# Kernel optimization log

Measured on AMD Instinct MI355X. Metric: run time of the kernel, lower is better.

The kernel has to match this reference:

```python
import jax, jax.numpy as jnp
import numpy as np

HIDDEN = 1024
HEADS = 16
HEAD_DIM = HIDDEN // HEADS
SCALE = HEAD_DIM ** (-0.5)


def setup_inputs() -> dict:
    key = jax.random.key(0)
    ks = jax.random.split(key, 5)
    B, N, C = 8, 1024, HIDDEN
    x = jax.random.normal(ks[0], (B, N, C), dtype=jnp.float32)
    # torch nn.Linear params: weight [out, in], bias [out]
    w_in = jax.random.normal(ks[1], (3 * C, C), dtype=jnp.float32) * (C ** -0.5)
    b_in = jax.random.normal(ks[2], (3 * C,), dtype=jnp.float32) * 0.02
    w_out = jax.random.normal(ks[3], (C, C), dtype=jnp.float32) * (C ** -0.5)
    b_out = jax.random.normal(ks[4], (C,), dtype=jnp.float32) * 0.02
    return {"x": x, "w_in": w_in, "b_in": b_in, "w_out": w_out, "b_out": b_out}


def reference(x, w_in, b_in, w_out, b_out):
    B, N, C = x.shape
    H, D = HEADS, HEAD_DIM
    # in_proj: [B,N,3C] -> (3,B,H,N,D)
    qkv = x @ w_in.T + b_in
    qkv = qkv.reshape(B, N, 3, H, D).transpose(2, 0, 3, 1, 4)
    q, k, v = qkv[0], qkv[1], qkv[2]
    # attention scores scaled after QK^T (same math as scaling q)
    attn = jnp.einsum("bhnd,bhmd->bhnm", q, k) * SCALE
    attn = jax.nn.softmax(attn, axis=-1)
    out = jnp.einsum("bhnm,bhmd->bhnd", attn, v)  # [B,H,N,D]
    out = out.transpose(0, 2, 1, 3).reshape(B, N, C)
    return out @ w_out.T + b_out
```

## Files before the change

kernel.cpp:

```cpp
#include <hip/hip_runtime.h>


typedef __attribute__((ext_vector_type(8))) __bf16 bf16x8;
typedef __attribute__((ext_vector_type(4))) __bf16 bf16x4;
typedef __attribute__((ext_vector_type(4))) float f32x4;
typedef __attribute__((ext_vector_type(4))) short short4v;

__device__ __forceinline__ f32x4 mfma16(bf16x8 a, bf16x8 b, f32x4 c) {
  return __builtin_amdgcn_mfma_f32_16x16x32_bf16(a, b, c, 0, 0, 0);
}

#if __has_builtin(__builtin_amdgcn_mfma_f32_16x16x16bf16_1k)
__device__ __forceinline__ f32x4 mfma_pv(bf16x4 a, bf16x4 b, f32x4 c) {
  short4v as = __builtin_bit_cast(short4v, a);
  short4v bs = __builtin_bit_cast(short4v, b);
  return __builtin_amdgcn_mfma_f32_16x16x16bf16_1k(as, bs, c, 0, 0, 0);
}
#else
__device__ __forceinline__ f32x4 mfma_pv(bf16x4 a, bf16x4 b, f32x4 c) {
  __bf16 z = (__bf16)0.f;
  bf16x8 a8 = {a[0], a[1], a[2], a[3], z, z, z, z};
  bf16x8 b8 = {b[0], b[1], b[2], b[3], z, z, z, z};
  return mfma16(a8, b8, c);
}
#endif

__device__ __forceinline__ float fexp2(float x) {
#if __has_builtin(__builtin_amdgcn_exp2f)
  return __builtin_amdgcn_exp2f(x);
#else
  return exp2f(x);
#endif
}

typedef __attribute__((address_space(1))) const unsigned int gu32;
typedef __attribute__((address_space(3))) unsigned int lu32;

__device__ __forceinline__ void async16(const void* g, void* l) {
  __builtin_amdgcn_global_load_lds((gu32*)g, (lu32*)l, 16, 0, 0);
}

__global__ __launch_bounds__(256) void cvt_all(const float* __restrict__ x,
                                               __bf16* __restrict__ xb,
                                               const float* __restrict__ wi,
                                               __bf16* __restrict__ wib,
                                               const float* __restrict__ wo,
                                               __bf16* __restrict__ wob) {
  int blk = blockIdx.x;
  const float* in;
  __bf16* out;
  int base;
  if (blk < 4096)      { in = x;  out = xb;  base = 0; }
  else if (blk < 5632) { in = wi; out = wib; base = 4096; }
  else                 { in = wo; out = wob; base = 5632; }
  int i = ((blk - base) * 256 + threadIdx.x) * 8;
  float4 a = *(const float4*)(in + i);
  float4 b = *(const float4*)(in + i + 4);
  bf16x8 o;
  o[0] = (__bf16)a.x; o[1] = (__bf16)a.y; o[2] = (__bf16)a.z; o[3] = (__bf16)a.w;
  o[4] = (__bf16)b.x; o[5] = (__bf16)b.y; o[6] = (__bf16)b.z; o[7] = (__bf16)b.w;
  *(bf16x8*)(out + i) = o;
}

template <int NB, bool WRITE_VT, typename OutT>
__global__ __launch_bounds__(256) void gemm_nt(const __bf16* __restrict__ A,
                                               const __bf16* __restrict__ Bm,
                                               const float* __restrict__ bias,
                                               OutT* __restrict__ C, int K, int ldc,
                                               __bf16* __restrict__ vt) {
  __shared__ __bf16 As[128 * 64];
  __shared__ __bf16 Bs[NB * 32 * 64];
  const int t = threadIdx.x;
  const int wv = t >> 6, lane = t & 63;
  const int q16 = lane & 15, quad = lane >> 4;
  const int wm = wv >> 1, wn = wv & 1;
  const long m0 = (long)blockIdx.x * 128;
  const long n0 = (long)blockIdx.y * (NB * 32);

  f32x4 zero = {0.f, 0.f, 0.f, 0.f};
  f32x4 acc[4][NB];
#pragma unroll
  for (int i = 0; i < 4; ++i)
#pragma unroll
    for (int j = 0; j < NB; ++j) acc[i][j] = zero;

  char* AsB = (char*)As;
  char* BsB = (char*)Bs;
  const int sr = t >> 3;
  const int gc = (t & 7) ^ (sr & 7);

  for (int kt = 0; kt < K; kt += 64) {
    __syncthreads();
#pragma unroll
    for (int i = 0; i < 4; ++i)
      async16(A + (m0 + i * 32 + sr) * K + kt + gc * 8, AsB + i * 4096 + wv * 1024);
#pragma unroll
    for (int i = 0; i < NB; ++i)
      async16(Bm + (n0 + i * 32 + sr) * K + kt + gc * 8, BsB + i * 4096 + wv * 1024);
    __syncthreads();

#pragma unroll
    for (int kk = 0; kk < 2; ++kk) {
      bf16x8 af[4], bf[NB];
#pragma unroll
      for (int i = 0; i < 4; ++i) {
        int ra = wm * 64 + i * 16 + q16;
        af[i] = *(const bf16x8*)(AsB + ra * 128 + (((kk * 4 + quad) ^ (ra & 7)) * 16));
      }
#pragma unroll
      for (int j = 0; j < NB; ++j) {
        int rb = wn * (NB * 16) + j * 16 + q16;
        bf[j] = *(const bf16x8*)(BsB + rb * 128 + (((kk * 4 + quad) ^ (rb & 7)) * 16));
      }
#pragma unroll
      for (int i = 0; i < 4; ++i)
#pragma unroll
        for (int j = 0; j < NB; ++j) acc[i][j] = mfma16(af[i], bf[j], acc[i][j]);
    }
  }

  if (WRITE_VT && n0 >= 2048) {
    const int b = (int)(m0 >> 10);
    const int nbase = (int)(m0 - (long)b * 1024) + wm * 64;
#pragma unroll
    for (int j = 0; j < NB; ++j) {
      int col = (int)n0 + wn * (NB * 16) + j * 16 + q16;
      int cc = col - 2048;
      int h = cc >> 6, d = cc & 63;
      float bs = bias[col];
      __bf16* vrow = vt + (((long)(b * 16 + h)) << 16) + (long)d * 1024;
#pragma unroll
      for (int i = 0; i < 4; ++i) {
        int n = nbase + i * 16 + quad * 4;
        bf16x4 o;
#pragma unroll
        for (int r = 0; r < 4; ++r) o[r] = (__bf16)(acc[i][j][r] + bs);
        *(bf16x4*)(vrow + n) = o;
      }
    }
  } else {
#pragma unroll
    for (int j = 0; j < NB; ++j) {
      long col = n0 + wn * (NB * 16) + j * 16 + q16;
      float bs = bias[col];
#pragma unroll
      for (int i = 0; i < 4; ++i) {
        long rowb = m0 + wm * 64 + i * 16 + quad * 4;
#pragma unroll
        for (int r = 0; r < 4; ++r) {
          float v = acc[i][j][r] + bs;
          C[(rowb + r) * (long)ldc + col] = (OutT)v;
        }
      }
    }
  }
}

template <typename OutT>
__global__ __launch_bounds__(256) void gemm_nt64(const __bf16* __restrict__ A,
                                                 const __bf16* __restrict__ Bm,
                                                 const float* __restrict__ bias,
                                                 OutT* __restrict__ C, int K, int ldc) {
  __shared__ __bf16 As[64 * 64];
  __shared__ __bf16 Bs[128 * 64];
  const int t = threadIdx.x;
  const int wv = t >> 6, lane = t & 63;
  const int q16 = lane & 15, quad = lane >> 4;
  const int wm = wv >> 1, wn = wv & 1;
  const long m0 = (long)blockIdx.x * 64;
  const long n0 = (long)blockIdx.y * 128;

  f32x4 zero = {0.f, 0.f, 0.f, 0.f};
  f32x4 acc[2][4];
#pragma unroll
  for (int i = 0; i < 2; ++i)
#pragma unroll
    for (int j = 0; j < 4; ++j) acc[i][j] = zero;

  char* AsB = (char*)As;
  char* BsB = (char*)Bs;
  const int sr = t >> 3;
  const int gc = (t & 7) ^ (sr & 7);

  for (int kt = 0; kt < K; kt += 64) {
    __syncthreads();
#pragma unroll
    for (int i = 0; i < 2; ++i)
      async16(A + (m0 + i * 32 + sr) * K + kt + gc * 8, AsB + i * 4096 + wv * 1024);
#pragma unroll
    for (int i = 0; i < 4; ++i)
      async16(Bm + (n0 + i * 32 + sr) * K + kt + gc * 8, BsB + i * 4096 + wv * 1024);
    __syncthreads();

#pragma unroll
    for (int kk = 0; kk < 2; ++kk) {
      bf16x8 af[2], bf[4];
#pragma unroll
      for (int i = 0; i < 2; ++i) {
        int ra = wm * 32 + i * 16 + q16;
        af[i] = *(const bf16x8*)(AsB + ra * 128 + (((kk * 4 + quad) ^ (ra & 7)) * 16));
      }
#pragma unroll
      for (int j = 0; j < 4; ++j) {
        int rb = wn * 64 + j * 16 + q16;
        bf[j] = *(const bf16x8*)(BsB + rb * 128 + (((kk * 4 + quad) ^ (rb & 7)) * 16));
      }
#pragma unroll
      for (int i = 0; i < 2; ++i)
#pragma unroll
        for (int j = 0; j < 4; ++j) acc[i][j] = mfma16(af[i], bf[j], acc[i][j]);
    }
  }

#pragma unroll
  for (int j = 0; j < 4; ++j) {
    long col = n0 + wn * 64 + j * 16 + q16;
    float bs = bias[col];
#pragma unroll
    for (int i = 0; i < 2; ++i) {
      long rowb = m0 + wm * 32 + i * 16 + quad * 4;
#pragma unroll
      for (int r = 0; r < 4; ++r) {
        float v = acc[i][j][r] + bs;
        C[(rowb + r) * (long)ldc + col] = (OutT)v;
      }
    }
  }
}

__global__ __launch_bounds__(256) void attn_kernel(const __bf16* __restrict__ qkv,
                                                   const __bf16* __restrict__ vt,
                                                   __bf16* __restrict__ ao) {
  __shared__ __bf16 Ks[64 * 64];
  __shared__ __bf16 Vt[64 * 64];
  const int t = threadIdx.x;
  const int wv = t >> 6, lane = t & 63;
  const int q16 = lane & 15, quad = lane >> 4;
  const int bh = blockIdx.x;
  const int b = bh >> 4, h = bh & 15;
  const int q0 = blockIdx.y * 64;
  const long rowbase = (long)b * 1024;

  bf16x8 qf0, qf1;
  {
    long qrow = rowbase + q0 + wv * 16 + q16;
    const __bf16* qp = qkv + qrow * 3072 + h * 64 + quad * 8;
    qf0 = *(const bf16x8*)qp;
    qf1 = *(const bf16x8*)(qp + 32);
#pragma unroll
    for (int j = 0; j < 8; ++j) {
      qf0[j] = (__bf16)((float)qf0[j] * 0.18033688f);
      qf1[j] = (__bf16)((float)qf1[j] * 0.18033688f);
    }
  }

  f32x4 zero = {0.f, 0.f, 0.f, 0.f};
  f32x4 oacc[4];
#pragma unroll
  for (int dt = 0; dt < 4; ++dt) oacc[dt] = zero;
  float lcol = 0.f;

  char* KsB = (char*)Ks;
  char* VtB = (char*)Vt;
  const int sr = t >> 3;
  const int sgc = (t & 7) ^ (sr & 7);
  const int sw = q16 & 7;

  for (int kv0 = 0; kv0 < 1024; kv0 += 64) {
    __syncthreads();
    const __bf16* kg = qkv + (rowbase + kv0 + sr) * 3072 + 1024 + h * 64 + sgc * 8;
    async16(kg, KsB + wv * 1024);
    async16(kg + (long)32 * 3072, KsB + 4096 + wv * 1024);
    const __bf16* vg = vt + (long)bh * 65536 + (long)sr * 1024 + kv0 + sgc * 8;
    async16(vg, VtB + wv * 1024);
    async16(vg + (long)32 * 1024, VtB + 4096 + wv * 1024);
    __syncthreads();

    f32x4 sacc[4];
#pragma unroll
    for (int nt = 0; nt < 4; ++nt) sacc[nt] = zero;
#pragma unroll
    for (int nt = 0; nt < 4; ++nt) {
      int kvr = nt * 16 + q16;
      bf16x8 kf0 = *(const bf16x8*)(KsB + kvr * 128 + ((quad ^ sw) * 16));
      bf16x8 kf1 = *(const bf16x8*)(KsB + kvr * 128 + (((4 + quad) ^ sw) * 16));
      sacc[nt] = mfma16(kf0, qf0, sacc[nt]);
      sacc[nt] = mfma16(kf1, qf1, sacc[nt]);
    }

    bf16x4 pf[4];
#pragma unroll
    for (int nt = 0; nt < 4; ++nt)
#pragma unroll
      for (int r = 0; r < 4; ++r) {
        float p = fexp2(sacc[nt][r]);
        lcol += p;
        pf[nt][r] = (__bf16)p;
      }

#pragma unroll
    for (int nt = 0; nt < 4; ++nt) {
      int c = ((nt * 2 + (quad >> 1)) ^ sw) * 16 + (quad & 1) * 8;
#pragma unroll
      for (int dt = 0; dt < 4; ++dt) {
        bf16x4 vf = *(const bf16x4*)(VtB + (dt * 16 + q16) * 128 + c);
        oacc[dt] = mfma_pv(pf[nt], vf, oacc[dt]);
      }
    }
  }

  lcol += __shfl_xor(lcol, 16);
  lcol += __shfl_xor(lcol, 32);
  float inv = 1.0f / lcol;
#pragma unroll
  for (int r = 0; r < 4; ++r) {
    float ir = __shfl(inv, quad * 4 + r);
    long orow = rowbase + q0 + wv * 16 + quad * 4 + r;
#pragma unroll
    for (int dt = 0; dt < 4; ++dt)
      ao[orow * 1024 + h * 64 + dt * 16 + q16] = (__bf16)(oacc[dt][r] * ir);
  }
}

extern "C" void kernel_launch(void* const* d_in, const int* in_sizes, int n_in,
                              void* d_out, int out_size, void* d_ws, size_t ws_size,
                              hipStream_t stream) {
  const float* x     = (const float*)d_in[0];
  const float* w_in  = (const float*)d_in[1];
  const float* b_in  = (const float*)d_in[2];
  const float* w_out = (const float*)d_in[3];
  const float* b_out = (const float*)d_in[4];
  float* out = (float*)d_out;

  char* ws = (char*)d_ws;
  __bf16* xb   = (__bf16*)(ws);
  __bf16* wib  = (__bf16*)(ws + 16777216);
  __bf16* wob  = (__bf16*)(ws + 23068672);
  __bf16* qkvb = (__bf16*)(ws + 25165824);
  __bf16* aob  = (__bf16*)(ws + 75497472);
  __bf16* vtg  = (__bf16*)d_out;

  cvt_all<<<6144, 256, 0, stream>>>(x, xb, w_in, wib, w_out, wob);
  gemm_nt<4, true, __bf16><<<dim3(64, 24), 256, 0, stream>>>(
      xb, wib, b_in, qkvb, 1024, 3072, vtg);
  attn_kernel<<<dim3(128, 16), 256, 0, stream>>>(qkvb, vtg, aob);
  gemm_nt64<float><<<dim3(128, 8), 256, 0, stream>>>(
      aob, wob, b_out, out, 1024, 1024);
}
```

Baseline: 243.9 us.

## Rewrite QKV projection GEMM as 256x256 double-buffered tile with prefetch

Replaces the 128x128-tile QKV GEMM with a 512-thread kernel that computes 256x256 output tiles. It double-buffers 128KB of LDS so the next K-slice loads asynchronously while MFMAs run, raises MFMA priority with setprio, and swizzles block order for L2 locality. The goal is to hide global load latency and cut operand re-reads. In exchange it uses far more LDS and registers per block, so occupancy drops, and only 384 blocks launch.

```diff
diff --git a/kernel.cpp b/kernel.cpp
--- a/kernel.cpp
+++ b/kernel.cpp
@@ -62,94 +62,131 @@
   *(bf16x8*)(out + i) = o;
 }
 
-template <int NB, bool WRITE_VT, typename OutT>
-__global__ __launch_bounds__(256) void gemm_nt(const __bf16* __restrict__ A,
-                                               const __bf16* __restrict__ Bm,
-                                               const float* __restrict__ bias,
-                                               OutT* __restrict__ C, int K, int ldc,
-                                               __bf16* __restrict__ vt) {
-  __shared__ __bf16 As[128 * 64];
-  __shared__ __bf16 Bs[NB * 32 * 64];
+template <bool WRITE_VT>
+__global__ __launch_bounds__(512, 2) void gemm256(const __bf16* __restrict__ A,
+                                                  const __bf16* __restrict__ Bm,
+                                                  const float* __restrict__ bias,
+                                                  __bf16* __restrict__ C,
+                                                  __bf16* __restrict__ vt) {
+  __shared__ char lds[131072];
   const int t = threadIdx.x;
   const int wv = t >> 6, lane = t & 63;
   const int q16 = lane & 15, quad = lane >> 4;
-  const int wm = wv >> 1, wn = wv & 1;
-  const long m0 = (long)blockIdx.x * 128;
-  const long n0 = (long)blockIdx.y * (NB * 32);
+  const int wm = wv >> 2, wn = wv & 3;
+
+  const int bid = blockIdx.x;
+  const int swz = (bid & 7) * 48 + (bid >> 3);
+  const long m0 = (long)(swz & 31) * 256;
+  const long n0 = (long)(swz >> 5) * 256;
+
+  const int sr = t >> 3;
+  const int sgc = (t & 7) ^ (sr & 7);
+  const int ldst = wv * 1024;
 
   f32x4 zero = {0.f, 0.f, 0.f, 0.f};
-  f32x4 acc[4][NB];
-#pragma unroll
-  for (int i = 0; i < 4; ++i)
-#pragma unroll
-    for (int j = 0; j < NB; ++j) acc[i][j] = zero;
-
-  char* AsB = (char*)As;
-  char* BsB = (char*)Bs;
-  const int sr = t >> 3;
-  const int gc = (t & 7) ^ (sr & 7);
-
-  for (int kt = 0; kt < K; kt += 64) {
-    __syncthreads();
-#pragma unroll
-    for (int i = 0; i < 4; ++i)
-      async16(A + (m0 + i * 32 + sr) * K + kt + gc * 8, AsB + i * 4096 + wv * 1024);
-#pragma unroll
-    for (int i = 0; i < NB; ++i)
-      async16(Bm + (n0 + i * 32 + sr) * K + kt + gc * 8, BsB + i * 4096 + wv * 1024);
-    __syncthreads();
-
+  f32x4 acc[8][4];
+#pragma unroll
+  for (int i = 0; i < 8; ++i)
+#pragma unroll
+    for (int j = 0; j < 4; ++j) acc[i][j] = zero;
+
+  {
+    char* A0 = lds;
+    char* B0 = lds + 32768;
+#pragma unroll
+    for (int i = 0; i < 4; ++i) {
+      async16(A + (m0 + i * 64 + sr) * 1024 + sgc * 8, A0 + i * 8192 + ldst);
+      async16(Bm + (n0 + i * 64 + sr) * 1024 + sgc * 8, B0 + i * 8192 + ldst);
+    }
+  }
+  asm volatile("s_waitcnt vmcnt(0)" ::);
+  __builtin_amdgcn_s_barrier();
+
+  int cur = 0;
+#pragma unroll 1
+  for (int kt = 0; kt < 1024; kt += 64) {
+    const bool pref = kt < 960;
+    char* Ac = lds + cur * 65536;
+    char* Bc = Ac + 32768;
+    char* An = lds + (cur ^ 1) * 65536;
+    char* Bn = An + 32768;
+    const int ktn = kt + 64;
+
+    bf16x8 bfr[4];
 #pragma unroll
     for (int kk = 0; kk < 2; ++kk) {
-      bf16x8 af[4], bf[NB];
-#pragma unroll
-      for (int i = 0; i < 4; ++i) {
-        int ra = wm * 64 + i * 16 + q16;
-        af[i] = *(const bf16x8*)(AsB + ra * 128 + (((kk * 4 + quad) ^ (ra & 7)) * 16));
-      }
-#pragma unroll
-      for (int j = 0; j < NB; ++j) {
-        int rb = wn * (NB * 16) + j * 16 + q16;
-        bf[j] = *(const bf16x8*)(BsB + rb * 128 + (((kk * 4 + quad) ^ (rb & 7)) * 16));
-      }
-#pragma unroll
-      for (int i = 0; i < 4; ++i)
-#pragma unroll
-        for (int j = 0; j < NB; ++j) acc[i][j] = mfma16(af[i], bf[j], acc[i][j]);
-    }
+#pragma unroll
+      for (int mh = 0; mh < 2; ++mh) {
+        bf16x8 af[4];
+#pragma unroll
+        for (int mi = 0; mi < 4; ++mi) {
+          int ra = wm * 128 + (mh * 4 + mi) * 16 + q16;
+          af[mi] = *(const bf16x8*)(Ac + ra * 128 + (((kk * 4 + quad) ^ (ra & 7)) * 16));
+        }
+        if (mh == 0) {
+#pragma unroll
+          for (int nj = 0; nj < 4; ++nj) {
+            int rb = wn * 64 + nj * 16 + q16;
+            bfr[nj] = *(const bf16x8*)(Bc + rb * 128 + (((kk * 4 + quad) ^ (rb & 7)) * 16));
+          }
+        }
+        if (pref && kk == 0) {
+          const int i0 = mh * 2, i1 = mh * 2 + 1;
+          async16(A + (m0 + i0 * 64 + sr) * 1024 + ktn + sgc * 8, An + i0 * 8192 + ldst);
+          async16(A + (m0 + i1 * 64 + sr) * 1024 + ktn + sgc * 8, An + i1 * 8192 + ldst);
+          async16(Bm + (n0 + i0 * 64 + sr) * 1024 + ktn + sgc * 8, Bn + i0 * 8192 + ldst);
+          async16(Bm + (n0 + i1 * 64 + sr) * 1024 + ktn + sgc * 8, Bn + i1 * 8192 + ldst);
+        }
+        __builtin_amdgcn_s_barrier();
+        __builtin_amdgcn_s_setprio(1);
+#pragma unroll
+        for (int mi = 0; mi < 4; ++mi)
+#pragma unroll
+          for (int nj = 0; nj < 4; ++nj)
+            acc[mh * 4 + mi][nj] = mfma16(af[mi], bfr[nj], acc[mh * 4 + mi][nj]);
+        __builtin_amdgcn_s_setprio(0);
+        __builtin_amdgcn_s_barrier();
+      }
+    }
+    if (pref) {
+      asm volatile("s_waitcnt vmcnt(0)" ::);
+      __builtin_amdgcn_sched_barrier(0);
+    }
+    __builtin_amdgcn_s_barrier();
+    cur ^= 1;
   }
 
   if (WRITE_VT && n0 >= 2048) {
     const int b = (int)(m0 >> 10);
-    const int nbase = (int)(m0 - (long)b * 1024) + wm * 64;
-#pragma unroll
-    for (int j = 0; j < NB; ++j) {
-      int col = (int)n0 + wn * (NB * 16) + j * 16 + q16;
+    const int nbase = (int)(m0 & 1023) + wm * 128;
+#pragma unroll
+    for (int nj = 0; nj < 4; ++nj) {
+      int col = (int)n0 + wn * 64 + nj * 16 + q16;
       int cc = col - 2048;
       int h = cc >> 6, d = cc & 63;
       float bs = bias[col];
       __bf16* vrow = vt + (((long)(b * 16 + h)) << 16) + (long)d * 1024;
 #pragma unroll
-      for (int i = 0; i < 4; ++i) {
-        int n = nbase + i * 16 + quad * 4;
+      for (int mi = 0; mi < 8; ++mi) {
+        int n = nbase + mi * 16 + quad * 4;
         bf16x4 o;
 #pragma unroll
-        for (int r = 0; r < 4; ++r) o[r] = (__bf16)(acc[i][j][r] + bs);
+        for (int r = 0; r < 4; ++r) o[r] = (__bf16)(acc[mi][nj][r] + bs);
         *(bf16x4*)(vrow + n) = o;
       }
     }
   } else {
 #pragma unroll
-    for (int j = 0; j < NB; ++j) {
-      long col = n0 + wn * (NB * 16) + j * 16 + q16;
+    for (int nj = 0; nj < 4; ++nj) {
+      long col = n0 + wn * 64 + nj * 16 + q16;
       float bs = bias[col];
 #pragma unroll
-      for (int i = 0; i < 4; ++i) {
-        long rowb = m0 + wm * 64 + i * 16 + quad * 4;
+      for (int mi = 0; mi < 8; ++mi) {
+        long rowb = m0 + wm * 128 + mi * 16 + quad * 4;
 #pragma unroll
         for (int r = 0; r < 4; ++r) {
-          float v = acc[i][j][r] + bs;
-          C[(rowb + r) * (long)ldc + col] = (OutT)v;
+          float v = acc[mi][nj][r] + bs;
+          C[(rowb + r) * 3072 + col] = (__bf16)v;
         }
       }
     }
@@ -341,8 +378,7 @@
   __bf16* vtg  = (__bf16*)d_out;
 
   cvt_all<<<6144, 256, 0, stream>>>(x, xb, w_in, wib, w_out, wob);
-  gemm_nt<4, true, __bf16><<<dim3(64, 24), 256, 0, stream>>>(
-      xb, wib, b_in, qkvb, 1024, 3072, vtg);
+  gemm256<true><<<384, 512, 0, stream>>>(xb, wib, b_in, qkvb, vtg);
   attn_kernel<<<dim3(128, 16), 256, 0, stream>>>(qkvb, vtg, aob);
   gemm_nt64<float><<<dim3(128, 8), 256, 0, stream>>>(
       aob, wob, b_out, out, 1024, 1024);
```

After: 248.0 us. No clear change (+1.7%).
